# Kernel tuning notes

Hardware: AMD Instinct MI355X
Metric: run time of the kernel (lower is better)

## Reference

```python
import jax, jax.numpy as jnp
import numpy as np

B, DIM, H, W = 2, 256, 32, 32
HALF, DI, DS, DTR = DIM // 2, 256, 16, 8
DEPTH, K1 = 2, 4


def _ln(x, w, b, eps=1e-5):
    m = jnp.mean(x, -1, keepdims=True)
    v = jnp.var(x, -1, keepdims=True)
    return (x - m) * jax.lax.rsqrt(v + eps) * w + b


def _selective_scan(dA, dBu, C):
    # dA, dBu: (N, L, D, S); C: (N, L, S) -> y: (N, L, D)
    def step(h, ab):
        a, b = ab
        h = a * h + b
        return h, h
    h0 = jnp.zeros((dA.shape[0],) + dA.shape[2:], dA.dtype)
    _, hs = jax.lax.scan(step, h0, (jnp.moveaxis(dA, 1, 0), jnp.moveaxis(dBu, 1, 0)))
    return jnp.einsum('lnds,nls->nld', hs, C)


def _mamba_block(xs, ln_w, ln_b, in_w, cw, cb, xw, dtw, dtb, Alog, Dp, ow):
    # xs: (B, L, HALF); canonical Mamba-1 block, pre-LN residual
    Lq = xs.shape[1]
    h = _ln(xs, ln_w, ln_b)
    u, z = jnp.split(h @ in_w, 2, axis=-1)  # (B,L,DI) each
    up = jnp.pad(u, ((0, 0), (K1 - 1, 0), (0, 0)))  # causal depthwise conv1d
    u = sum(up[:, k:k + Lq, :] * cw[:, k] for k in range(K1)) + cb
    u = jax.nn.silu(u)
    dbc = u @ xw
    dtr, Bm, Cm = jnp.split(dbc, [DTR, DTR + DS], axis=-1)
    dt = jax.nn.softplus(dtr @ dtw + dtb)  # (B,L,DI)
    A = -jnp.exp(Alog)  # (DI,DS)
    dA = jnp.exp(dt[..., None] * A)
    dBu = (dt * u)[..., None] * Bm[:, :, None, :]
    y = _selective_scan(dA, dBu, Cm) + u * Dp
    return xs + (y * jax.nn.silu(z)) @ ow


def _vss_block(x, ln_w, ln_b, in_w, cw, cb, xw, dtw, dtb, Alog, Dp, on_w, on_b, ow):
    # x: (B, HALF, H, W); VMamba SS2D block (4-direction cross-scan), pre-LN residual
    Bq, _, Hq, Wq = x.shape
    Lq = Hq * Wq
    h = _ln(x.transpose(0, 2, 3, 1), ln_w, ln_b)
    u, z = jnp.split(h @ in_w, 2, axis=-1)  # (B,H,W,DI)
    u2 = jax.lax.conv_general_dilated(u.transpose(0, 3, 1, 2), cw[:, None], (1, 1), ((1, 1), (1, 1)),
                                      feature_group_count=DI,
                                      dimension_numbers=('NCHW', 'OIHW', 'NCHW')) + cb[None, :, None, None]
    u2 = jax.nn.silu(u2)  # (B,DI,H,W)
    s0 = u2.reshape(Bq, DI, Lq)
    s1 = u2.transpose(0, 1, 3, 2).reshape(Bq, DI, Lq)
    us = jnp.stack([s0, s1, jnp.flip(s0, -1), jnp.flip(s1, -1)], 1).transpose(0, 1, 3, 2)  # (B,4,L,DI)
    dbc = jnp.einsum('bkld,kdr->bklr', us, xw)
    dtr, Bm, Cm = jnp.split(dbc, [DTR, DTR + DS], axis=-1)
    dt = jax.nn.softplus(jnp.einsum('bklr,krd->bkld', dtr, dtw) + dtb[None, :, None, :])
    A = -jnp.exp(Alog)  # (4,DI,DS)
    dA = jnp.exp(dt[..., None] * A[None, :, None])  # (B,4,L,DI,DS)
    dBu = (dt * us)[..., None] * Bm[:, :, :, None, :]
    y = _selective_scan(dA.reshape(Bq * 4, Lq, DI, DS), dBu.reshape(Bq * 4, Lq, DI, DS), Cm.reshape(Bq * 4, Lq, DS))
    y = y.reshape(Bq, 4, Lq, DI) + us * Dp[None, :, None, :]
    yt = y.transpose(0, 1, 3, 2)  # (B,4,DI,L)
    y0 = yt[:, 0]
    y1 = yt[:, 1].reshape(Bq, DI, Wq, Hq).transpose(0, 1, 3, 2).reshape(Bq, DI, Lq)
    y2 = jnp.flip(yt[:, 2], -1)
    y3 = jnp.flip(yt[:, 3], -1).reshape(Bq, DI, Wq, Hq).transpose(0, 1, 3, 2).reshape(Bq, DI, Lq)
    ym = _ln((y0 + y1 + y2 + y3).transpose(0, 2, 1), on_w, on_b)  # (B,L,DI)
    out = (ym * jax.nn.silu(z.reshape(Bq, Lq, DI))) @ ow  # (B,L,HALF)
    return x + out.reshape(Bq, Hq, Wq, HALF).transpose(0, 3, 1, 2)


def _fwd(x, proj1_w, proj1_b, proj2_w, proj2_b,
         m_ln_w, m_ln_b, m_in_w, m_conv_w, m_conv_b, m_xproj_w, m_dt_w, m_dt_b, m_Alog, m_D, m_out_w,
         v_ln_w, v_ln_b, v_in_w, v_conv_w, v_conv_b, v_xproj_w, v_dt_w, v_dt_b, v_Alog, v_D,
         v_onorm_w, v_onorm_b, v_out_w, fuse_w, fuse_b, bn_g, bn_b, bn_m, bn_v):
    Bq, _, Hq, Wq = x.shape
    Lq = Hq * Wq
    p1 = jnp.einsum('oc,bchw->bohw', proj1_w, x) + proj1_b[None, :, None, None]
    s = p1.reshape(Bq, HALF, Lq).transpose(0, 2, 1)
    for i in range(DEPTH):
        s = _mamba_block(s, m_ln_w[i], m_ln_b[i], m_in_w[i], m_conv_w[i], m_conv_b[i], m_xproj_w[i],
                         m_dt_w[i], m_dt_b[i], m_Alog[i], m_D[i], m_out_w[i])
    p1 = s.transpose(0, 2, 1).reshape(Bq, HALF, Hq, Wq)
    p2 = jnp.einsum('oc,bchw->bohw', proj2_w, x) + proj2_b[None, :, None, None]
    for i in range(DEPTH):
        p2 = _vss_block(p2, v_ln_w[i], v_ln_b[i], v_in_w[i], v_conv_w[i], v_conv_b[i], v_xproj_w[i],
                        v_dt_w[i], v_dt_b[i], v_Alog[i], v_D[i], v_onorm_w[i], v_onorm_b[i], v_out_w[i])
    xc = jnp.concatenate([p1, p2], 1)
    y = jax.lax.conv_general_dilated(xc, fuse_w, (1, 1), ((1, 1), (1, 1)),
                                     dimension_numbers=('NCHW', 'OIHW', 'NCHW')) + fuse_b[None, :, None, None]
    y = (y - bn_m[None, :, None, None]) * jax.lax.rsqrt(bn_v + 1e-5)[None, :, None, None] * bn_g[None, :, None, None] + bn_b[None, :, None, None]
    return jax.nn.relu(y)


def setup_inputs() -> dict:
    key = jax.random.key(0)
    ks = iter(jax.random.split(key, 64))
    n = lambda shape, s=0.02: jax.random.normal(next(ks), shape, jnp.float32) * s
    A_row = jnp.log(jnp.arange(1, DS + 1, dtype=jnp.float32))  # standard S4D-real init
    return {
        'x': jax.random.normal(next(ks), (B, DIM, H, W), jnp.float32),
        'proj1_w': n((HALF, DIM), 0.05), 'proj1_b': n((HALF,)),
        'proj2_w': n((HALF, DIM), 0.05), 'proj2_b': n((HALF,)),
        'm_ln_w': jnp.ones((DEPTH, HALF)), 'm_ln_b': jnp.zeros((DEPTH, HALF)),
        'm_in_w': n((DEPTH, HALF, 2 * DI)),
        'm_conv_w': n((DEPTH, DI, K1), 0.1), 'm_conv_b': n((DEPTH, DI)),
        'm_xproj_w': n((DEPTH, DI, DTR + 2 * DS)),
        'm_dt_w': n((DEPTH, DTR, DI), 0.1), 'm_dt_b': n((DEPTH, DI)),
        'm_Alog': jnp.array(jnp.broadcast_to(A_row, (DEPTH, DI, DS))),
        'm_D': jnp.ones((DEPTH, DI)),
        'm_out_w': n((DEPTH, DI, HALF)),
        'v_ln_w': jnp.ones((DEPTH, HALF)), 'v_ln_b': jnp.zeros((DEPTH, HALF)),
        'v_in_w': n((DEPTH, HALF, 2 * DI)),
        'v_conv_w': n((DEPTH, DI, 3, 3), 0.1), 'v_conv_b': n((DEPTH, DI)),
        'v_xproj_w': n((DEPTH, 4, DI, DTR + 2 * DS)),
        'v_dt_w': n((DEPTH, 4, DTR, DI), 0.1), 'v_dt_b': n((DEPTH, 4, DI)),
        'v_Alog': jnp.array(jnp.broadcast_to(A_row, (DEPTH, 4, DI, DS))),
        'v_D': jnp.ones((DEPTH, 4, DI)),
        'v_onorm_w': jnp.ones((DEPTH, DI)), 'v_onorm_b': jnp.zeros((DEPTH, DI)),
        'v_out_w': n((DEPTH, DI, HALF)),
        'fuse_w': n((DIM, DIM, 3, 3), 0.02), 'fuse_b': n((DIM,)),
        'bn_g': jnp.ones((DIM,)), 'bn_b': jnp.zeros((DIM,)),
        'bn_m': n((DIM,)), 'bn_v': jax.random.uniform(next(ks), (DIM,), jnp.float32, 0.5, 1.5),
    }


def reference(x, proj1_w, proj1_b, proj2_w, proj2_b,
              m_ln_w, m_ln_b, m_in_w, m_conv_w, m_conv_b, m_xproj_w, m_dt_w, m_dt_b, m_Alog, m_D, m_out_w,
              v_ln_w, v_ln_b, v_in_w, v_conv_w, v_conv_b, v_xproj_w, v_dt_w, v_dt_b, v_Alog, v_D,
              v_onorm_w, v_onorm_b, v_out_w, fuse_w, fuse_b, bn_g, bn_b, bn_m, bn_v):
    return _fwd(x, proj1_w, proj1_b, proj2_w, proj2_b,
                m_ln_w, m_ln_b, m_in_w, m_conv_w, m_conv_b, m_xproj_w, m_dt_w, m_dt_b, m_Alog, m_D, m_out_w,
                v_ln_w, v_ln_b, v_in_w, v_conv_w, v_conv_b, v_xproj_w, v_dt_w, v_dt_b, v_Alog, v_D,
                v_onorm_w, v_onorm_b, v_out_w, fuse_w, fuse_b, bn_g, bn_b, bn_m, bn_v)
```

## Files before the change

### kernel.cpp

```cpp
#include <hip/hip_runtime.h>
#include <math.h>

#define CH  16
#define NCH 64

typedef __attribute__((ext_vector_type(8))) short bf16x8;
typedef __attribute__((ext_vector_type(4))) float f32x4;
typedef __attribute__((ext_vector_type(4))) unsigned int u32x4;

__device__ __forceinline__ float dev_silu(float x){ return x * (1.0f/(1.0f + __expf(-x))); }
__device__ __forceinline__ float dev_softplus(float x){ return fmaxf(x,0.0f) + log1pf(__expf(-fabsf(x))); }
__device__ __forceinline__ unsigned short dev_bf16(float f){
    unsigned int u = __float_as_uint(f);
    return (unsigned short)((u + 0x7fffu + ((u >> 16) & 1u)) >> 16);
}

__global__ void __launch_bounds__(256)
k_prep(const float* __restrict__ w1, const float* __restrict__ w2, float* __restrict__ wtc,
       const float* __restrict__ fw, unsigned short* __restrict__ Wr)
{
    if (blockIdx.x < 64){
        int bc = blockIdx.x;
        int ot = bc & 7, ct = bc >> 3;
        __shared__ float t[32][33];
        int col = threadIdx.x & 31, r8 = threadIdx.x >> 5;
        #pragma unroll
        for (int i = 0; i < 4; ++i){
            int r = i*8 + r8;
            int o = ot*32 + r;
            const float* src = (o < 128) ? (w1 + (size_t)o*256) : (w2 + (size_t)(o-128)*256);
            t[r][col] = src[ct*32 + col];
        }
        __syncthreads();
        #pragma unroll
        for (int i = 0; i < 4; ++i){
            int r = i*8 + r8;
            int c = ct*32 + r, o = ot*32 + col;
            wtc[(size_t)c*256 + o] = t[col][r];
        }
    } else {
        int t0 = ((blockIdx.x - 64)*256 + threadIdx.x)*4;
        unsigned int r[4];
        #pragma unroll
        for (int j = 0; j < 4; ++j){
            int i = t0 + j;
            int o = i / 2304, kk = i - o*2304;
            int kp = kk >> 8, cc = kk & 255;
            r[j] = dev_bf16(fw[(size_t)o*2304 + cc*9 + kp]);
        }
        uint2 pk; pk.x = r[0] | (r[1] << 16); pk.y = r[2] | (r[3] << 16);
        *(uint2*)(Wr + t0) = pk;
    }
}

__global__ void __launch_bounds__(256)
k_proj(const float* __restrict__ x, const float* __restrict__ wtc,
       const float* __restrict__ b1, const float* __restrict__ b2,
       float* __restrict__ sm, float* __restrict__ sv)
{
    int blk = blockIdx.x;
    int b = blk >> 8, l0 = (blk & 255) * 4;
    int tid = threadIdx.x;
    __shared__ float4 xs[256];
    xs[tid] = *(const float4*)(x + ((size_t)(b*256 + tid))*1024 + l0);
    __syncthreads();
    int o = tid & 127;
    float bias = (tid < 128) ? b1[o] : b2[o];
    float a0 = bias, a1 = bias, a2 = bias, a3 = bias;
    #pragma unroll 4
    for (int c = 0; c < 256; ++c){
        float wv = wtc[(size_t)c*256 + tid];
        float4 xv = xs[c];
        a0 = fmaf(wv, xv.x, a0);
        a1 = fmaf(wv, xv.y, a1);
        a2 = fmaf(wv, xv.z, a2);
        a3 = fmaf(wv, xv.w, a3);
    }
    float* dst = (tid < 128) ? sm : sv;
    size_t base = ((size_t)b*1024 + l0)*128 + o;
    dst[base      ] = a0;
    dst[base + 128] = a1;
    dst[base + 256] = a2;
    dst[base + 384] = a3;
}

__device__ __forceinline__ void lnmm_core(int bl0, float4 v,
    const float* __restrict__ lnw, const float* __restrict__ lnb,
    const float* __restrict__ inw, float* __restrict__ u, float* __restrict__ z,
    float (*hn)[132])
{
    int tid = threadIdx.x;
    int row = tid >> 5, lane = tid & 31;
    float a = v.x + v.y + v.z + v.w;
    float q = v.x*v.x + v.y*v.y + v.z*v.z + v.w*v.w;
    #pragma unroll
    for (int o = 16; o; o >>= 1){ a += __shfl_xor(a, o); q += __shfl_xor(q, o); }
    float mean = a * (1.0f/128.0f);
    float rs = rsqrtf(q * (1.0f/128.0f) - mean*mean + 1e-5f);
    float4 w4 = *(const float4*)(lnw + lane*4);
    float4 b4 = *(const float4*)(lnb + lane*4);
    float4 hv;
    hv.x = (v.x-mean)*rs*w4.x + b4.x;
    hv.y = (v.y-mean)*rs*w4.y + b4.y;
    hv.z = (v.z-mean)*rs*w4.z + b4.z;
    hv.w = (v.w-mean)*rs*w4.w + b4.w;
    *(float4*)&hn[row][lane*4] = hv;
    __syncthreads();
    float acc0[8] = {0,0,0,0,0,0,0,0};
    float acc1[8] = {0,0,0,0,0,0,0,0};
    for (int c = 0; c < 128; c += 4){
        float w0[4], w1[4];
        #pragma unroll
        for (int i = 0; i < 4; ++i){
            w0[i] = inw[(size_t)(c+i)*512 + tid];
            w1[i] = inw[(size_t)(c+i)*512 + tid + 256];
        }
        #pragma unroll
        for (int r = 0; r < 8; ++r){
            float4 h4 = *(const float4*)&hn[r][c];
            acc0[r] = fmaf(h4.x, w0[0], acc0[r]);
            acc0[r] = fmaf(h4.y, w0[1], acc0[r]);
            acc0[r] = fmaf(h4.z, w0[2], acc0[r]);
            acc0[r] = fmaf(h4.w, w0[3], acc0[r]);
            acc1[r] = fmaf(h4.x, w1[0], acc1[r]);
            acc1[r] = fmaf(h4.y, w1[1], acc1[r]);
            acc1[r] = fmaf(h4.z, w1[2], acc1[r]);
            acc1[r] = fmaf(h4.w, w1[3], acc1[r]);
        }
    }
    #pragma unroll
    for (int r = 0; r < 8; ++r){
        u[(size_t)(bl0 + r)*256 + tid] = acc0[r];
        z[(size_t)(bl0 + r)*256 + tid] = acc1[r];
    }
}

__global__ void __launch_bounds__(256)
k_lnmm2(const float* __restrict__ sm_, const float* __restrict__ mlnw, const float* __restrict__ mlnb,
        const float* __restrict__ minw, float* __restrict__ um, float* __restrict__ zm,
        const float* __restrict__ sv_, const float* __restrict__ vlnw, const float* __restrict__ vlnb,
        const float* __restrict__ vinw, float* __restrict__ uv, float* __restrict__ zv)
{
    __shared__ float hn[8][132];
    int tid = threadIdx.x;
    int row = tid >> 5, lane = tid & 31;
    if (blockIdx.x < 256){
        int bl0 = blockIdx.x*8;
        float4 v = *(const float4*)(sm_ + (size_t)(bl0 + row)*128 + lane*4);
        lnmm_core(bl0, v, mlnw, mlnb, minw, um, zm, hn);
    } else {
        int bl0 = (blockIdx.x-256)*8;
        float4 v = *(const float4*)(sv_ + (size_t)(bl0 + row)*128 + lane*4);
        lnmm_core(bl0, v, vlnw, vlnb, vinw, uv, zv, hn);
    }
}

__global__ void __launch_bounds__(256)
k_conv2(const float* __restrict__ urm, const float* __restrict__ cwm, const float* __restrict__ cbm,
        float* __restrict__ uc,
        const float* __restrict__ urv, const float* __restrict__ cwv, const float* __restrict__ cbv,
        float* __restrict__ us)
{
    int d = threadIdx.x;
    if (blockIdx.x < 2048){
        int bl = blockIdx.x; int b = bl >> 10, l = bl & 1023;
        float acc = cbm[d];
        #pragma unroll
        for (int k = 0; k < 4; ++k){
            int lp = l - 3 + k;
            if (lp >= 0) acc = fmaf(urm[((size_t)(b<<10) + lp)*256 + d], cwm[d*4 + k], acc);
        }
        uc[(size_t)bl*256 + d] = dev_silu(acc);
    } else {
        int bl = blockIdx.x - 2048; int b = bl >> 10, l = bl & 1023;
        int h = l >> 5, w = l & 31;
        float acc = cbv[d];
        #pragma unroll
        for (int kh = 0; kh < 3; ++kh){
            int hh = h + kh - 1; if (hh < 0 || hh > 31) continue;
            #pragma unroll
            for (int kw = 0; kw < 3; ++kw){
                int ww = w + kw - 1; if (ww < 0 || ww > 31) continue;
                acc = fmaf(urv[((size_t)(b<<10) + (hh<<5) + ww)*256 + d], cwv[d*9 + kh*3 + kw], acc);
            }
        }
        float v = dev_silu(acc);
        int l1 = (w<<5) + h;
        size_t base = (size_t)b*4*1024*256;
        us[base + ((size_t)0*1024 + l        )*256 + d] = v;
        us[base + ((size_t)1*1024 + l1       )*256 + d] = v;
        us[base + ((size_t)2*1024 + (1023-l ))*256 + d] = v;
        us[base + ((size_t)3*1024 + (1023-l1))*256 + d] = v;
    }
}

__device__ __forceinline__ void xproj_body(size_t idx0, int k, const float* __restrict__ u,
    const float* __restrict__ xw, const float* __restrict__ dtw, const float* __restrict__ dtb,
    float* __restrict__ dt, float* __restrict__ Bm, float* __restrict__ Cm)
{
    int tid = threadIdx.x;
    __shared__ float ursh[4][256];
    __shared__ float dbc[4][44];
    #pragma unroll
    for (int p = 0; p < 4; ++p)
        ursh[p][tid] = u[(idx0 + p)*256 + tid];
    __syncthreads();
    if (tid < 160){
        int r = tid % 40, p = tid / 40;
        const float* xwc = xw + (size_t)k*256*40 + r;
        float a0 = 0.f, a1 = 0.f;
        for (int c = 0; c < 128; ++c){
            a0 = fmaf(ursh[p][c],       xwc[(size_t)c*40],       a0);
            a1 = fmaf(ursh[p][c + 128], xwc[(size_t)(c+128)*40], a1);
        }
        dbc[p][r] = a0 + a1;
    }
    __syncthreads();
    const float* dtwk = dtw + (size_t)k*8*256;
    float bias = dtb[k*256 + tid];
    float wv[8];
    #pragma unroll
    for (int r = 0; r < 8; ++r) wv[r] = dtwk[r*256 + tid];
    #pragma unroll
    for (int p = 0; p < 4; ++p){
        float a = bias;
        #pragma unroll
        for (int r = 0; r < 8; ++r) a = fmaf(dbc[p][r], wv[r], a);
        dt[(idx0 + p)*256 + tid] = dev_softplus(a);
    }
    if (tid < 128){
        int p = tid >> 5, j = tid & 31;
        if (j < 16) Bm[(idx0 + p)*16 + j]        = dbc[p][8 + j];
        else        Cm[(idx0 + p)*16 + (j - 16)] = dbc[p][8 + j];
    }
}

__global__ void __launch_bounds__(256)
k_xproj2(const float* __restrict__ um, const float* __restrict__ mxw, const float* __restrict__ mdtw,
         const float* __restrict__ mdtb, float* __restrict__ dtm, float* __restrict__ Bmm,
         float* __restrict__ Cmm,
         const float* __restrict__ uv, const float* __restrict__ vxw, const float* __restrict__ vdtw,
         const float* __restrict__ vdtb, float* __restrict__ dtv, float* __restrict__ Bmv,
         float* __restrict__ Cmv)
{
    if (blockIdx.x < 512){
        int bk = blockIdx.x >> 8;
        size_t idx0 = (size_t)bk*1024 + (blockIdx.x & 255)*4;
        xproj_body(idx0, 0, um, mxw, mdtw, mdtb, dtm, Bmm, Cmm);
    } else {
        int blk = blockIdx.x - 512;
        int bk = blk >> 8;
        size_t idx0 = (size_t)bk*1024 + (blk & 255)*4;
        xproj_body(idx0, bk & 3, uv, vxw, vdtw, vdtb, dtv, Bmv, Cmv);
    }
}

__device__ __forceinline__ void scanA_body(int bk, int c, int k, const float* __restrict__ dt,
    const float* __restrict__ u, const float* __restrict__ Bm, const float* __restrict__ Alog,
    float* __restrict__ Pb, float* __restrict__ Qb)
{
    int d = threadIdx.x;
    __shared__ float Bsh[CH][16];
    {
        int j = threadIdx.x >> 4, s = threadIdx.x & 15;
        Bsh[j][s] = Bm[((size_t)bk*1024 + c*CH + j)*16 + s];
    }
    float dtv[CH], duv[CH];
    size_t base = ((size_t)bk*1024 + c*CH)*256 + d;
    #pragma unroll
    for (int j = 0; j < CH; ++j){
        float a = dt[base + (size_t)j*256];
        float b = u [base + (size_t)j*256];
        dtv[j] = a; duv[j] = a*b;
    }
    float A[16];
    const float4* Ap = (const float4*)(Alog + ((size_t)k*256 + d)*16);
    #pragma unroll
    for (int q = 0; q < 4; ++q){
        float4 v = Ap[q];
        A[q*4+0] = -__expf(v.x); A[q*4+1] = -__expf(v.y);
        A[q*4+2] = -__expf(v.z); A[q*4+3] = -__expf(v.w);
    }
    __syncthreads();
    float Q[16];
    #pragma unroll
    for (int s = 0; s < 16; ++s) Q[s] = 0.f;
    float S = 0.f;
    #pragma unroll
    for (int j = 0; j < CH; ++j){
        S += dtv[j];
        #pragma unroll
        for (int s = 0; s < 16; ++s){
            float av = __expf(dtv[j]*A[s]);
            Q[s] = fmaf(av, Q[s], duv[j]*Bsh[j][s]);
        }
    }
    size_t oidx = ((size_t)(bk*NCH + c)*256 + d)*16;
    float4* Pp = (float4*)(Pb + oidx);
    float4* Qp = (float4*)(Qb + oidx);
    #pragma unroll
    for (int q = 0; q < 4; ++q){
        float4 pv, qv;
        pv.x = __expf(S*A[q*4+0]); pv.y = __expf(S*A[q*4+1]);
        pv.z = __expf(S*A[q*4+2]); pv.w = __expf(S*A[q*4+3]);
        qv.x = Q[q*4+0]; qv.y = Q[q*4+1]; qv.z = Q[q*4+2]; qv.w = Q[q*4+3];
        Pp[q] = pv; Qp[q] = qv;
    }
}

__global__ void __launch_bounds__(256)
k_scanA2(const float* __restrict__ dtm, const float* __restrict__ um, const float* __restrict__ Bmm,
         const float* __restrict__ mAlog, float* __restrict__ Pbm, float* __restrict__ Qbm,
         const float* __restrict__ dtv, const float* __restrict__ uv, const float* __restrict__ Bmv,
         const float* __restrict__ vAlog, float* __restrict__ Pbv, float* __restrict__ Qbv)
{
    if (blockIdx.x < 128){
        int blk = blockIdx.x;
        scanA_body(blk >> 6, blk & (NCH-1), 0, dtm, um, Bmm, mAlog, Pbm, Qbm);
    } else {
        int blk = blockIdx.x - 128;
        int bk = blk >> 6;
        scanA_body(bk, blk & (NCH-1), bk & 3, dtv, uv, Bmv, vAlog, Pbv, Qbv);
    }
}

__device__ __forceinline__ void scanP_body(int bk, int dg, float* __restrict__ Pb,
                                           const float* __restrict__ Qb)
{
    int tid = threadIdx.x;
    size_t idx0 = (size_t)bk*NCH*4096 + dg*256 + tid;
    float Pv[NCH], Qv[NCH];
    #pragma unroll
    for (int c = 0; c < NCH; ++c){
        Pv[c] = Pb[idx0 + (size_t)c*4096];
        Qv[c] = Qb[idx0 + (size_t)c*4096];
    }
    float h = 0.f;
    #pragma unroll
    for (int c = 0; c < NCH; ++c){
        Pb[idx0 + (size_t)c*4096] = h;
        h = fmaf(Pv[c], h, Qv[c]);
    }
}

__global__ void __launch_bounds__(256)
k_scanP2(float* __restrict__ Pbm, const float* __restrict__ Qbm,
         float* __restrict__ Pbv, const float* __restrict__ Qbv)
{
    if (blockIdx.x < 32) scanP_body(blockIdx.x >> 4, blockIdx.x & 15, Pbm, Qbm);
    else { int blk = blockIdx.x - 32; scanP_body(blk >> 4, blk & 15, Pbv, Qbv); }
}

__device__ __forceinline__ void scanB_body(int bk, int c, int k, const float* __restrict__ dt,
    const float* __restrict__ u, const float* __restrict__ Bm, const float* __restrict__ Cm,
    const float* __restrict__ Alog, const float* __restrict__ Hb, float* __restrict__ y)
{
    int d = threadIdx.x;
    __shared__ float Bsh[CH][16], Csh[CH][16];
    {
        int j = threadIdx.x >> 4, s = threadIdx.x & 15;
        size_t bi = ((size_t)bk*1024 + c*CH + j)*16 + s;
        Bsh[j][s] = Bm[bi];
        Csh[j][s] = Cm[bi];
    }
    float dtv[CH], duv[CH];
    size_t base = ((size_t)bk*1024 + c*CH)*256 + d;
    #pragma unroll
    for (int j = 0; j < CH; ++j){
        float a = dt[base + (size_t)j*256];
        float b = u [base + (size_t)j*256];
        dtv[j] = a; duv[j] = a*b;
    }
    float A[16];
    const float4* Ap = (const float4*)(Alog + ((size_t)k*256 + d)*16);
    #pragma unroll
    for (int q = 0; q < 4; ++q){
        float4 v = Ap[q];
        A[q*4+0] = -__expf(v.x); A[q*4+1] = -__expf(v.y);
        A[q*4+2] = -__expf(v.z); A[q*4+3] = -__expf(v.w);
    }
    float h[16];
    const float4* Hp = (const float4*)(Hb + ((size_t)(bk*NCH + c)*256 + d)*16);
    #pragma unroll
    for (int q = 0; q < 4; ++q){
        float4 v = Hp[q];
        h[q*4+0] = v.x; h[q*4+1] = v.y; h[q*4+2] = v.z; h[q*4+3] = v.w;
    }
    __syncthreads();
    float* yp = y + base;
    #pragma unroll
    for (int j = 0; j < CH; ++j){
        float py = 0.f;
        #pragma unroll
        for (int s = 0; s < 16; ++s){
            float av = __expf(dtv[j]*A[s]);
            h[s] = fmaf(av, h[s], duv[j]*Bsh[j][s]);
            py = fmaf(h[s], Csh[j][s], py);
        }
        yp[(size_t)j*256] = py;
    }
}

__global__ void __launch_bounds__(256)
k_scanB2(const float* __restrict__ dtm, const float* __restrict__ um, const float* __restrict__ Bmm,
         const float* __restrict__ Cmm, const float* __restrict__ mAlog,
         const float* __restrict__ Hbm, float* __restrict__ ym,
         const float* __restrict__ dtv, const float* __restrict__ uv, const float* __restrict__ Bmv,
         const float* __restrict__ Cmv, const float* __restrict__ vAlog,
         const float* __restrict__ Hbv, float* __restrict__ yv)
{
    if (blockIdx.x < 128){
        int blk = blockIdx.x;
        scanB_body(blk >> 6, blk & (NCH-1), 0, dtm, um, Bmm, Cmm, mAlog, Hbm, ym);
    } else {
        int blk = blockIdx.x - 128;
        int bk = blk >> 6;
        scanB_body(bk, blk & (NCH-1), bk & 3, dtv, uv, Bmv, Cmv, vAlog, Hbv, yv);
    }
}

__device__ __forceinline__ void mout_body(int bl0, const float* __restrict__ y,
    const float* __restrict__ uc, const float* __restrict__ z, const float* __restrict__ Dp,
    const float* __restrict__ ow, float* __restrict__ sm)
{
    int tid = threadIdx.x;
    int row = tid >> 5, c0 = (tid & 31) * 8;
    __shared__ float gld[8][264];
    size_t base = (size_t)(bl0 + row)*256 + c0;
    #pragma unroll
    for (int i = 0; i < 8; i += 4){
        float4 yv = *(const float4*)(y + base + i);
        float4 uv = *(const float4*)(uc + base + i);
        float4 zv = *(const float4*)(z + base + i);
        float4 dv = *(const float4*)(Dp + c0 + i);
        gld[row][c0+i+0] = (yv.x + uv.x*dv.x) * dev_silu(zv.x);
        gld[row][c0+i+1] = (yv.y + uv.y*dv.y) * dev_silu(zv.y);
        gld[row][c0+i+2] = (yv.z + uv.z*dv.z) * dev_silu(zv.z);
        gld[row][c0+i+3] = (yv.w + uv.w*dv.w) * dev_silu(zv.w);
    }
    __syncthreads();
    int o = tid & 127, rg = tid >> 7;
    float acc[4] = {0,0,0,0};
    for (int c = 0; c < 256; c += 4){
        float w[4];
        #pragma unroll
        for (int i = 0; i < 4; ++i) w[i] = ow[(size_t)(c+i)*128 + o];
        #pragma unroll
        for (int r = 0; r < 4; ++r){
            float4 h4 = *(const float4*)&gld[rg*4 + r][c];
            acc[r] = fmaf(h4.x, w[0], acc[r]);
            acc[r] = fmaf(h4.y, w[1], acc[r]);
            acc[r] = fmaf(h4.z, w[2], acc[r]);
            acc[r] = fmaf(h4.w, w[3], acc[r]);
        }
    }
    #pragma unroll
    for (int r = 0; r < 4; ++r)
        sm[(size_t)(bl0 + rg*4 + r)*128 + o] += acc[r];
}

__device__ __forceinline__ void vcomb_body(int blk, const float* __restrict__ y,
    const float* __restrict__ us, const float* __restrict__ z, const float* __restrict__ Dp,
    const float* __restrict__ onw, const float* __restrict__ onb, const float* __restrict__ ow,
    float* __restrict__ sv)
{
    int b = blk >> 7;
    int l0 = (blk & 127) * 8;
    int tid = threadIdx.x;
    int row = tid >> 5, c0 = (tid & 31) * 8;
    int l = l0 + row;
    int h = l >> 5, w = l & 31;
    int l1 = (w<<5) + h, l2 = 1023 - l, l3 = 1023 - l1;
    size_t base = (size_t)b*4*1024*256;
    size_t i0 = base + ((size_t)0*1024 + l )*256 + c0;
    size_t i1 = base + ((size_t)1*1024 + l1)*256 + c0;
    size_t i2 = base + ((size_t)2*1024 + l2)*256 + c0;
    size_t i3 = base + ((size_t)3*1024 + l3)*256 + c0;
    float t[8];
    #pragma unroll
    for (int i = 0; i < 8; i += 4){
        float4 yv = *(const float4*)(y + i0 + i);
        float4 uv = *(const float4*)(us + i0 + i);
        float4 dv = *(const float4*)(Dp + 0*256 + c0 + i);
        t[i+0] = yv.x + uv.x*dv.x; t[i+1] = yv.y + uv.y*dv.y;
        t[i+2] = yv.z + uv.z*dv.z; t[i+3] = yv.w + uv.w*dv.w;
    }
    #pragma unroll
    for (int i = 0; i < 8; i += 4){
        float4 yv = *(const float4*)(y + i1 + i);
        float4 uv = *(const float4*)(us + i1 + i);
        float4 dv = *(const float4*)(Dp + 1*256 + c0 + i);
        t[i+0] += yv.x + uv.x*dv.x; t[i+1] += yv.y + uv.y*dv.y;
        t[i+2] += yv.z + uv.z*dv.z; t[i+3] += yv.w + uv.w*dv.w;
    }
    #pragma unroll
    for (int i = 0; i < 8; i += 4){
        float4 yv = *(const float4*)(y + i2 + i);
        float4 uv = *(const float4*)(us + i2 + i);
        float4 dv = *(const float4*)(Dp + 2*256 + c0 + i);
        t[i+0] += yv.x + uv.x*dv.x; t[i+1] += yv.y + uv.y*dv.y;
        t[i+2] += yv.z + uv.z*dv.z; t[i+3] += yv.w + uv.w*dv.w;
    }
    #pragma unroll
    for (int i = 0; i < 8; i += 4){
        float4 yv = *(const float4*)(y + i3 + i);
        float4 uv = *(const float4*)(us + i3 + i);
        float4 dv = *(const float4*)(Dp + 3*256 + c0 + i);
        t[i+0] += yv.x + uv.x*dv.x; t[i+1] += yv.y + uv.y*dv.y;
        t[i+2] += yv.z + uv.z*dv.z; t[i+3] += yv.w + uv.w*dv.w;
    }
    float a = 0.f, q = 0.f;
    #pragma unroll
    for (int i = 0; i < 8; ++i){ a += t[i]; q += t[i]*t[i]; }
    #pragma unroll
    for (int o = 16; o; o >>= 1){ a += __shfl_xor(a, o); q += __shfl_xor(q, o); }
    float mean = a * (1.0f/256.0f);
    float rs = rsqrtf(q * (1.0f/256.0f) - mean*mean + 1e-5f);
    __shared__ float gld[8][264];
    size_t zbase = (size_t)(b*1024 + l)*256 + c0;
    #pragma unroll
    for (int i = 0; i < 8; i += 4){
        float4 wv = *(const float4*)(onw + c0 + i);
        float4 bv = *(const float4*)(onb + c0 + i);
        float4 zv = *(const float4*)(z + zbase + i);
        gld[row][c0+i+0] = ((t[i+0]-mean)*rs*wv.x + bv.x) * dev_silu(zv.x);
        gld[row][c0+i+1] = ((t[i+1]-mean)*rs*wv.y + bv.y) * dev_silu(zv.y);
        gld[row][c0+i+2] = ((t[i+2]-mean)*rs*wv.z + bv.z) * dev_silu(zv.z);
        gld[row][c0+i+3] = ((t[i+3]-mean)*rs*wv.w + bv.w) * dev_silu(zv.w);
    }
    __syncthreads();
    int o = tid & 127, rg = tid >> 7;
    float acc[4] = {0,0,0,0};
    for (int c = 0; c < 256; c += 4){
        float wv[4];
        #pragma unroll
        for (int i = 0; i < 4; ++i) wv[i] = ow[(size_t)(c+i)*128 + o];
        #pragma unroll
        for (int r = 0; r < 4; ++r){
            float4 h4 = *(const float4*)&gld[rg*4 + r][c];
            acc[r] = fmaf(h4.x, wv[0], acc[r]);
            acc[r] = fmaf(h4.y, wv[1], acc[r]);
            acc[r] = fmaf(h4.z, wv[2], acc[r]);
            acc[r] = fmaf(h4.w, wv[3], acc[r]);
        }
    }
    #pragma unroll
    for (int r = 0; r < 4; ++r)
        sv[(size_t)(b*1024 + l0 + rg*4 + r)*128 + o] += acc[r];
}

__global__ void __launch_bounds__(256)
k_epi2(const float* __restrict__ ym, const float* __restrict__ uc, const float* __restrict__ zm,
       const float* __restrict__ mD, const float* __restrict__ mow, float* __restrict__ sm,
       const float* __restrict__ yv, const float* __restrict__ us, const float* __restrict__ zv,
       const float* __restrict__ vD, const float* __restrict__ onw, const float* __restrict__ onb,
       const float* __restrict__ vow, float* __restrict__ sv)
{
    if (blockIdx.x < 256) mout_body(blockIdx.x*8, ym, uc, zm, mD, mow, sm);
    else                  vcomb_body(blockIdx.x-256, yv, us, zv, vD, onw, onb, vow, sv);
}

__global__ void __launch_bounds__(256)
k_im2col(const float* __restrict__ sm, const float* __restrict__ sv,
         unsigned short* __restrict__ Bt)
{
    int n = blockIdx.x; int b = n >> 10, p = n & 1023;
    int h = p >> 5, w = p & 31;
    int tid = threadIdx.x;
    const float* src = (tid < 128) ? sm : sv;
    int c = tid & 127;
    #pragma unroll
    for (int kp = 0; kp < 9; ++kp){
        int kh = kp / 3, kw = kp - kh*3;
        int hh = h + kh - 1, ww = w + kw - 1;
        float v = 0.f;
        if ((unsigned)hh < 32u && (unsigned)ww < 32u)
            v = src[((size_t)b*1024 + (hh<<5) + ww)*128 + c];
        Bt[(size_t)n*2304 + kp*256 + tid] = dev_bf16(v);
    }
}

__global__ void __launch_bounds__(256)
k_fgemm(const unsigned short* __restrict__ Wr, const unsigned short* __restrict__ Bt,
        const float* __restrict__ fb, const float* __restrict__ bg, const float* __restrict__ bb,
        const float* __restrict__ bm, const float* __restrict__ bv, float* __restrict__ out)
{
    int o0 = (blockIdx.x & 3) * 64;
    int n0 = (blockIdx.x >> 2) * 64;
    int tid = threadIdx.x, lane = tid & 63, wid = tid >> 6;
    int wm = (wid >> 1) * 32, wn = (wid & 1) * 32;
    __shared__ unsigned short sA[64*40];
    __shared__ unsigned short sB[64*40];
    f32x4 acc[2][2] = {};
    int srow = tid >> 2, scol = (tid & 3) * 8;
    const u32x4* gA = (const u32x4*)(Wr + (size_t)(o0 + srow)*2304 + scol);
    const u32x4* gB = (const u32x4*)(Bt + (size_t)(n0 + srow)*2304 + scol);
    u32x4* wA = (u32x4*)(sA + srow*40 + scol);
    u32x4* wB = (u32x4*)(sB + srow*40 + scol);
    int fr = lane & 15, fk = (lane >> 4) * 8;
    const unsigned short* rA0 = sA + (wm + fr)*40 + fk;
    const unsigned short* rA1 = sA + (wm + 16 + fr)*40 + fk;
    const unsigned short* rB0 = sB + (wn + fr)*40 + fk;
    const unsigned short* rB1 = sB + (wn + 16 + fr)*40 + fk;
    for (int kt = 0; kt < 72; ++kt){
        u32x4 va = gA[kt*4];
        u32x4 vb = gB[kt*4];
        __syncthreads();
        *wA = va; *wB = vb;
        __syncthreads();
        bf16x8 a0 = *(const bf16x8*)rA0;
        bf16x8 a1 = *(const bf16x8*)rA1;
        bf16x8 b0 = *(const bf16x8*)rB0;
        bf16x8 b1 = *(const bf16x8*)rB1;
        acc[0][0] = __builtin_amdgcn_mfma_f32_16x16x32_bf16(a0, b0, acc[0][0], 0, 0, 0);
        acc[0][1] = __builtin_amdgcn_mfma_f32_16x16x32_bf16(a0, b1, acc[0][1], 0, 0, 0);
        acc[1][0] = __builtin_amdgcn_mfma_f32_16x16x32_bf16(a1, b0, acc[1][0], 0, 0, 0);
        acc[1][1] = __builtin_amdgcn_mfma_f32_16x16x32_bf16(a1, b1, acc[1][1], 0, 0, 0);
    }
    #pragma unroll
    for (int i = 0; i < 2; ++i){
        int ob = o0 + wm + i*16 + (lane >> 4) * 4;
        #pragma unroll
        for (int j = 0; j < 2; ++j){
            int n = n0 + wn + j*16 + (lane & 15);
            int b = n >> 10, p = n & 1023;
            #pragma unroll
            for (int q = 0; q < 4; ++q){
                int o = ob + q;
                float v = acc[i][j][q] + fb[o];
                v = (v - bm[o]) * rsqrtf(bv[o] + 1e-5f) * bg[o] + bb[o];
                out[((size_t)(b*256 + o))*1024 + p] = fmaxf(v, 0.f);
            }
        }
    }
}

extern "C" void kernel_launch(void* const* d_in, const int* in_sizes, int n_in,
                              void* d_out, int out_size, void* d_ws, size_t ws_size,
                              hipStream_t stream)
{
    const float* x         = (const float*)d_in[0];
    const float* proj1_w   = (const float*)d_in[1];
    const float* proj1_b   = (const float*)d_in[2];
    const float* proj2_w   = (const float*)d_in[3];
    const float* proj2_b   = (const float*)d_in[4];
    const float* m_ln_w    = (const float*)d_in[5];
    const float* m_ln_b    = (const float*)d_in[6];
    const float* m_in_w    = (const float*)d_in[7];
    const float* m_conv_w  = (const float*)d_in[8];
    const float* m_conv_b  = (const float*)d_in[9];
    const float* m_xproj_w = (const float*)d_in[10];
    const float* m_dt_w    = (const float*)d_in[11];
    const float* m_dt_b    = (const float*)d_in[12];
    const float* m_Alog    = (const float*)d_in[13];
    const float* m_D       = (const float*)d_in[14];
    const float* m_out_w   = (const float*)d_in[15];
    const float* v_ln_w    = (const float*)d_in[16];
    const float* v_ln_b    = (const float*)d_in[17];
    const float* v_in_w    = (const float*)d_in[18];
    const float* v_conv_w  = (const float*)d_in[19];
    const float* v_conv_b  = (const float*)d_in[20];
    const float* v_xproj_w = (const float*)d_in[21];
    const float* v_dt_w    = (const float*)d_in[22];
    const float* v_dt_b    = (const float*)d_in[23];
    const float* v_Alog    = (const float*)d_in[24];
    const float* v_D       = (const float*)d_in[25];
    const float* v_onorm_w = (const float*)d_in[26];
    const float* v_onorm_b = (const float*)d_in[27];
    const float* v_out_w   = (const float*)d_in[28];
    const float* fuse_w    = (const float*)d_in[29];
    const float* fuse_b    = (const float*)d_in[30];
    const float* bn_g      = (const float*)d_in[31];
    const float* bn_b      = (const float*)d_in[32];
    const float* bn_m      = (const float*)d_in[33];
    const float* bn_v      = (const float*)d_in[34];
    float* out = (float*)d_out;

    float* ws = (float*)d_ws;
    float* sm     = ws;  ws += 2*1024*128;
    float* sv     = ws;  ws += 2*1024*128;
    float* uraw_m = ws;  ws += 2*1024*256;
    float* zb_m   = ws;  ws += 2*1024*256;
    float* uc     = ws;  ws += 2*1024*256;
    float* uraw_v = ws;  ws += 2*1024*256;
    float* zb_v   = ws;  ws += 2*1024*256;
    float* usb    = ws;  ws += 2*4*1024*256;
    float* dt_m   = ws;  ws += 2*1024*256;
    float* yb_m   = ws;  ws += 2*1024*256;
    float* Pb_m   = ws;  ws += 2*NCH*256*16;
    float* Qb_m   = ws;  ws += 2*NCH*256*16;
    float* Bm_m   = ws;  ws += 2*1024*16;
    float* Cm_m   = ws;  ws += 2*1024*16;
    float* dt_v   = ws;  ws += 2*4*1024*256;
    float* yb_v   = ws;  ws += 2*4*1024*256;
    float* Pb_v   = ws;  ws += 2*4*NCH*256*16;
    float* Qb_v   = ws;  ws += 2*4*NCH*256*16;
    float* Bm_v   = ws;  ws += 2*4*1024*16;
    float* Cm_v   = ws;  ws += 2*4*1024*16;
    float* wtc    = ws;  ws += 256*256;
    unsigned short* Wr = (unsigned short*)ws;  ws += 576*1024/2;
    unsigned short* Bmat = (unsigned short*)dt_v;

    k_prep<<<640,   256, 0, stream>>>(proj1_w, proj2_w, wtc, fuse_w, Wr);
    k_proj<<<2*256, 256, 0, stream>>>(x, wtc, proj1_b, proj2_b, sm, sv);

    for (int i = 0; i < 2; ++i){
        k_lnmm2 <<<512,  256, 0, stream>>>(sm, m_ln_w + i*128, m_ln_b + i*128,
                                           m_in_w + (size_t)i*65536, uraw_m, zb_m,
                                           sv, v_ln_w + i*128, v_ln_b + i*128,
                                           v_in_w + (size_t)i*65536, uraw_v, zb_v);
        k_conv2 <<<4096, 256, 0, stream>>>(uraw_m, m_conv_w + (size_t)i*1024, m_conv_b + i*256, uc,
                                           uraw_v, v_conv_w + (size_t)i*2304, v_conv_b + i*256, usb);
        k_xproj2<<<2560, 256, 0, stream>>>(uc,  m_xproj_w + (size_t)i*10240,
                                           m_dt_w + (size_t)i*2048, m_dt_b + i*256,
                                           dt_m, Bm_m, Cm_m,
                                           usb, v_xproj_w + (size_t)i*40960,
                                           v_dt_w + (size_t)i*8192, v_dt_b + (size_t)i*1024,
                                           dt_v, Bm_v, Cm_v);
        k_scanA2<<<640,  256, 0, stream>>>(dt_m, uc,  Bm_m, m_Alog + (size_t)i*4096,  Pb_m, Qb_m,
                                           dt_v, usb, Bm_v, v_Alog + (size_t)i*16384, Pb_v, Qb_v);
        k_scanP2<<<160,  256, 0, stream>>>(Pb_m, Qb_m, Pb_v, Qb_v);
        k_scanB2<<<640,  256, 0, stream>>>(dt_m, uc,  Bm_m, Cm_m, m_Alog + (size_t)i*4096,
                                           Pb_m, yb_m,
                                           dt_v, usb, Bm_v, Cm_v, v_Alog + (size_t)i*16384,
                                           Pb_v, yb_v);
        k_epi2  <<<512,  256, 0, stream>>>(yb_m, uc, zb_m, m_D + i*256,
                                           m_out_w + (size_t)i*32768, sm,
                                           yb_v, usb, zb_v, v_D + (size_t)i*1024,
                                           v_onorm_w + i*256, v_onorm_b + i*256,
                                           v_out_w + (size_t)i*32768, sv);
    }

    k_im2col<<<2*1024, 256, 0, stream>>>(sm, sv, Bmat);
    k_fgemm <<<4*32,   256, 0, stream>>>(Wr, Bmat, fuse_b, bn_g, bn_b, bn_m, bn_v, out);
}
```

Baseline: 296.1 us.

## Fuse chunk-prefix scan into scanA via last-block atomic counter

```diff
diff --git a/kernel.cpp b/kernel.cpp
--- a/kernel.cpp
+++ b/kernel.cpp
@@ -241,8 +241,9 @@
          float* __restrict__ Cmm,
          const float* __restrict__ uv, const float* __restrict__ vxw, const float* __restrict__ vdtw,
          const float* __restrict__ vdtb, float* __restrict__ dtv, float* __restrict__ Bmv,
-         float* __restrict__ Cmv)
-{
+         float* __restrict__ Cmv, int* __restrict__ cnt)
+{
+    if (blockIdx.x == 0 && threadIdx.x < 16) cnt[threadIdx.x] = 0;
     if (blockIdx.x < 512){
         int bk = blockIdx.x >> 8;
         size_t idx0 = (size_t)bk*1024 + (blockIdx.x & 255)*4;
@@ -255,6 +256,27 @@
     }
 }
 
+__device__ __forceinline__ void scanP_body(int bk, int dg, float* __restrict__ Pb,
+                                           const float* __restrict__ Qb)
+{
+    int tid = threadIdx.x;
+    size_t idx0 = (size_t)bk*NCH*4096 + dg*256 + tid;
+    float h = 0.f;
+    for (int c0 = 0; c0 < NCH; c0 += 16){
+        float Pv[16], Qv[16];
+        #pragma unroll
+        for (int j = 0; j < 16; ++j){
+            Pv[j] = Pb[idx0 + (size_t)(c0+j)*4096];
+            Qv[j] = Qb[idx0 + (size_t)(c0+j)*4096];
+        }
+        #pragma unroll
+        for (int j = 0; j < 16; ++j){
+            Pb[idx0 + (size_t)(c0+j)*4096] = h;
+            h = fmaf(Pv[j], h, Qv[j]);
+        }
+    }
+}
+
 __device__ __forceinline__ void scanA_body(int bk, int c, int k, const float* __restrict__ dt,
     const float* __restrict__ u, const float* __restrict__ Bm, const float* __restrict__ Alog,
     float* __restrict__ Pb, float* __restrict__ Qb)
@@ -312,43 +334,32 @@
 k_scanA2(const float* __restrict__ dtm, const float* __restrict__ um, const float* __restrict__ Bmm,
          const float* __restrict__ mAlog, float* __restrict__ Pbm, float* __restrict__ Qbm,
          const float* __restrict__ dtv, const float* __restrict__ uv, const float* __restrict__ Bmv,
-         const float* __restrict__ vAlog, float* __restrict__ Pbv, float* __restrict__ Qbv)
-{
+         const float* __restrict__ vAlog, float* __restrict__ Pbv, float* __restrict__ Qbv,
+         int* __restrict__ cnt)
+{
+    int bk, cntIdx;
+    float *Pb, *Qb;
     if (blockIdx.x < 128){
         int blk = blockIdx.x;
-        scanA_body(blk >> 6, blk & (NCH-1), 0, dtm, um, Bmm, mAlog, Pbm, Qbm);
+        bk = blk >> 6;
+        scanA_body(bk, blk & (NCH-1), 0, dtm, um, Bmm, mAlog, Pbm, Qbm);
+        Pb = Pbm; Qb = Qbm; cntIdx = bk;
     } else {
         int blk = blockIdx.x - 128;
-        int bk = blk >> 6;
+        bk = blk >> 6;
         scanA_body(bk, blk & (NCH-1), bk & 3, dtv, uv, Bmv, vAlog, Pbv, Qbv);
-    }
-}
-
-__device__ __forceinline__ void scanP_body(int bk, int dg, float* __restrict__ Pb,
-                                           const float* __restrict__ Qb)
-{
-    int tid = threadIdx.x;
-    size_t idx0 = (size_t)bk*NCH*4096 + dg*256 + tid;
-    float Pv[NCH], Qv[NCH];
-    #pragma unroll
-    for (int c = 0; c < NCH; ++c){
-        Pv[c] = Pb[idx0 + (size_t)c*4096];
-        Qv[c] = Qb[idx0 + (size_t)c*4096];
-    }
-    float h = 0.f;
-    #pragma unroll
-    for (int c = 0; c < NCH; ++c){
-        Pb[idx0 + (size_t)c*4096] = h;
-        h = fmaf(Pv[c], h, Qv[c]);
-    }
-}
-
-__global__ void __launch_bounds__(256)
-k_scanP2(float* __restrict__ Pbm, const float* __restrict__ Qbm,
-         float* __restrict__ Pbv, const float* __restrict__ Qbv)
-{
-    if (blockIdx.x < 32) scanP_body(blockIdx.x >> 4, blockIdx.x & 15, Pbm, Qbm);
-    else { int blk = blockIdx.x - 32; scanP_body(blk >> 4, blk & 15, Pbv, Qbv); }
+        Pb = Pbv; Qb = Qbv; cntIdx = 2 + bk;
+    }
+    __shared__ int sdone;
+    __threadfence();
+    __syncthreads();
+    if (threadIdx.x == 0) sdone = atomicAdd(&cnt[cntIdx], 1);
+    __syncthreads();
+    if (sdone == NCH - 1){
+        __threadfence();
+        for (int dg = 0; dg < 16; ++dg)
+            scanP_body(bk, dg, Pb, Qb);
+    }
 }
 
 __device__ __forceinline__ void scanB_body(int bk, int c, int k, const float* __restrict__ dt,
@@ -699,6 +710,7 @@
     float* Cm_v   = ws;  ws += 2*4*1024*16;
     float* wtc    = ws;  ws += 256*256;
     unsigned short* Wr = (unsigned short*)ws;  ws += 576*1024/2;
+    int* cnt = (int*)ws;  ws += 16;
     unsigned short* Bmat = (unsigned short*)dt_v;
 
     k_prep<<<640,   256, 0, stream>>>(proj1_w, proj2_w, wtc, fuse_w, Wr);
@@ -716,10 +728,10 @@
                                            dt_m, Bm_m, Cm_m,
                                            usb, v_xproj_w + (size_t)i*40960,
                                            v_dt_w + (size_t)i*8192, v_dt_b + (size_t)i*1024,
-                                           dt_v, Bm_v, Cm_v);
+                                           dt_v, Bm_v, Cm_v, cnt);
         k_scanA2<<<640,  256, 0, stream>>>(dt_m, uc,  Bm_m, m_Alog + (size_t)i*4096,  Pb_m, Qb_m,
-                                           dt_v, usb, Bm_v, v_Alog + (size_t)i*16384, Pb_v, Qb_v);
-        k_scanP2<<<160,  256, 0, stream>>>(Pb_m, Qb_m, Pb_v, Qb_v);
+                                           dt_v, usb, Bm_v, v_Alog + (size_t)i*16384, Pb_v, Qb_v,
+                                           cnt);
         k_scanB2<<<640,  256, 0, stream>>>(dt_m, uc,  Bm_m, Cm_m, m_Alog + (size_t)i*4096,
                                            Pb_m, yb_m,
                                            dt_v, usb, Bm_v, Cm_v, v_Alog + (size_t)i*16384,
```

Result: slower. 606.4 us (+104.8%).
